# Optimization experiments

Hardware: AMD Instinct MI355X
Metric: run time of the kernel (lower is better)

The kernel has to match this reference:

```python
import jax, jax.numpy as jnp
import numpy as np

N_SPECIES = 2
N_RBF = 16
HIDDEN = 64
CUTOFF = 2.5


def setup_inputs() -> dict:
    key = jax.random.key(0)
    ks = jax.random.split(key, 10)
    B, N = 8, 1024
    positions = jax.random.uniform(ks[0], (B, N, 3), dtype=jnp.float32) * 10.0
    types = jax.random.randint(ks[1], (B, N), 0, N_SPECIES)
    in_dim = N_SPECIES + N_SPECIES * N_RBF  # 34
    def lin(k, fan_in, fan_out):
        bound = 1.0 / np.sqrt(fan_in)
        kw, kb = jax.random.split(k)
        W = jax.random.uniform(kw, (fan_in, fan_out), minval=-bound, maxval=bound, dtype=jnp.float32)
        b = jax.random.uniform(kb, (fan_out,), minval=-bound, maxval=bound, dtype=jnp.float32)
        return W, b
    W1, b1 = lin(ks[2], in_dim, 64)
    W2, b2 = lin(ks[3], 64, 64)
    W3, b3 = lin(ks[4], 64, HIDDEN)
    return {"positions": positions, "types": types,
            "W1": W1, "b1": b1, "W2": W2, "b2": b2, "W3": W3, "b3": b3}


def _forward(positions, types, W1, b1, W2, b2, W3, b3):
    B, N, _ = positions.shape
    # pairwise distances with safe sqrt (zero grad on diagonal, matching torch norm subgradient)
    disp = positions[:, :, None, :] - positions[:, None, :, :]          # [B,N,N,3]
    sq = jnp.sum(disp * disp, axis=-1)                                   # [B,N,N]
    nz = sq > 0.0
    d = jnp.sqrt(jnp.where(nz, sq, 1.0)) * nz
    # RBF expansion
    centers = jnp.linspace(0.0, CUTOFF, N_RBF)
    widths = jnp.full((N_RBF,), CUTOFF / max(N_RBF - 1, 1))
    diff = d[..., None] - centers                                        # [B,N,N,R]
    rbf = jnp.exp(-(diff ** 2) / (widths ** 2 + 1e-12))
    # smooth polynomial cutoff
    x = d / CUTOFF
    cut = jnp.where(d < CUTOFF, 1.0 - 6.0 * x ** 5 + 15.0 * x ** 4 - 10.0 * x ** 3, 0.0)
    rbf = rbf * cut[..., None]
    eye = jnp.eye(N, dtype=bool)[None, :, :, None]
    rbf = jnp.where(eye, 0.0, rbf)
    # species-weighted neighbor aggregation
    onehot = jax.nn.one_hot(types, N_SPECIES, dtype=positions.dtype)      # [B,N,S]
    env = jnp.einsum('bijr,bjs->birs', rbf, onehot).reshape(B, N, -1)     # [B,N,R*S]
    feats = jnp.concatenate([onehot, env], axis=-1)                       # [B,N,S+S*R]
    h = jax.nn.silu(feats @ W1 + b1)
    h = jax.nn.silu(h @ W2 + b2)
    return h @ W3 + b3                                                    # [B,N,HIDDEN]


def reference(positions, types, W1, b1, W2, b2, W3, b3):
    return _forward(positions, types, W1, b1, W2, b2, W3, b3)
```

## Files before the change

### kernel.cpp

```cpp
#include <hip/hip_runtime.h>
#include <hip/hip_bf16.h>

#define NTHREADS 256
#define N_ATOMS 1024
#define HIDDEN 64

__device__ __forceinline__ float rdlane(float v, int l) {
    return __int_as_float(__builtin_amdgcn_readlane(__float_as_int(v), l));
}

__global__ __launch_bounds__(NTHREADS) void LocalFeatureEncoder_40063454937486_kernel(
    const float* __restrict__ pos,
    const int*   __restrict__ types,
    const float* __restrict__ W1,
    const float* __restrict__ b1,
    const float* __restrict__ W2,
    const float* __restrict__ b2,
    const float* __restrict__ W3,
    const float* __restrict__ b3,
    float*       __restrict__ out)
{
    const int tid  = threadIdx.x;
    const int lane = tid & 63;
    const int a    = blockIdx.x * 4 + (tid >> 6);
    const int bidx = a >> 10;
    const int i    = a & (N_ATOMS - 1);

    const float* posb = pos + (size_t)bidx * N_ATOMS * 3;
    const int*   typb = types + (size_t)bidx * N_ATOMS;

    const float xi = posb[i * 3 + 0];
    const float yi = posb[i * 3 + 1];
    const float zi = posb[i * 3 + 2];

    const int   r16 = lane & 15;
    const int   slot = lane >> 4;
    const float c    = (float)r16 * (2.5f / 15.0f);

    float acc0 = 0.0f;
    float acc1 = 0.0f;

#pragma unroll
    for (int sweep = 0; sweep < N_ATOMS / 64; ++sweep) {
        const int j = lane + sweep * 64;
        const float px = posb[j * 3 + 0];
        const float py = posb[j * 3 + 1];
        const float pz = posb[j * 3 + 2];
        const int   tj = typb[j];
        const float dx = xi - px, dy = yi - py, dz = zi - pz;
        const float sq = dx * dx + dy * dy + dz * dz;
        const bool  pred = (j != i) && (sq < 6.25f);

        float dv = 0.0f, mp = 0.0f;
        if (pred) {
            const float d  = sqrtf(sq);
            const float x  = d * 0.4f;
            const float x3 = x * x * x;
            const float cutv = 1.0f + x3 * (-10.0f + x * (15.0f - 6.0f * x));
            dv = d;
            mp = (tj == 0) ? cutv : -cutv;
        }

        unsigned long long mask = __ballot(pred);
        while (mask) {
            float dA = 0.0f, mA = 0.0f, dB = 0.0f, mB = 0.0f;
            float dC = 0.0f, mC = 0.0f, dD = 0.0f, mD = 0.0f;
            {
                const int s = __builtin_ctzll(mask); mask &= mask - 1;
                dA = rdlane(dv, s); mA = rdlane(mp, s);
            }
            if (mask) {
                const int s = __builtin_ctzll(mask); mask &= mask - 1;
                dB = rdlane(dv, s); mB = rdlane(mp, s);
            }
            if (mask) {
                const int s = __builtin_ctzll(mask); mask &= mask - 1;
                dC = rdlane(dv, s); mC = rdlane(mp, s);
            }
            if (mask) {
                const int s = __builtin_ctzll(mask); mask &= mask - 1;
                dD = rdlane(dv, s); mD = rdlane(mp, s);
            }
            const float d = (slot == 0) ? dA : (slot == 1) ? dB : (slot == 2) ? dC : dD;
            const float m = (slot == 0) ? mA : (slot == 1) ? mB : (slot == 2) ? mC : dD == dD ? mD : mD;
            const float diff = d - c;
            const float e = __expf(diff * diff * -36.0f);
            acc0 += e * fmaxf(m, 0.0f);
            acc1 += e * fmaxf(-m, 0.0f);
        }
    }

    acc0 += __shfl_xor(acc0, 16, 64);
    acc0 += __shfl_xor(acc0, 32, 64);
    acc1 += __shfl_xor(acc1, 16, 64);
    acc1 += __shfl_xor(acc1, 32, 64);

    const int t  = lane;
    const int ti = typb[i];

    float h1 = b1[t] + W1[ti * HIDDEN + t];
#pragma unroll
    for (int r = 0; r < 16; ++r) {
        h1 += rdlane(acc0, r) * W1[(2 + 2 * r + 0) * HIDDEN + t];
        h1 += rdlane(acc1, r) * W1[(2 + 2 * r + 1) * HIDDEN + t];
    }
    h1 = h1 / (1.0f + __expf(-h1));

    float h2 = b2[t];
#pragma unroll
    for (int k = 0; k < HIDDEN; ++k) {
        h2 += rdlane(h1, k) * W2[k * HIDDEN + t];
    }
    h2 = h2 / (1.0f + __expf(-h2));

    float o = b3[t];
#pragma unroll
    for (int k = 0; k < HIDDEN; ++k) {
        o += rdlane(h2, k) * W3[k * HIDDEN + t];
    }
    out[(size_t)a * HIDDEN + t] = o;
}

extern "C" void kernel_launch(void* const* d_in, const int* in_sizes, int n_in,
                              void* d_out, int out_size, void* d_ws, size_t ws_size,
                              hipStream_t stream) {
    const float* pos   = (const float*)d_in[0];
    const int*   types = (const int*)d_in[1];
    const float* W1    = (const float*)d_in[2];
    const float* b1    = (const float*)d_in[3];
    const float* W2    = (const float*)d_in[4];
    const float* b2    = (const float*)d_in[5];
    const float* W3    = (const float*)d_in[6];
    const float* b3    = (const float*)d_in[7];
    float*       out   = (float*)d_out;

    const int BN = in_sizes[1];

    LocalFeatureEncoder_40063454937486_kernel<<<BN / 4, NTHREADS, 0, stream>>>(
        pos, types, W1, b1, W2, b2, W3, b3, out);
}
```

Measured before the change: 95.55 us.

## Split env and MLP kernels, stage positions in LDS, compact neighbors via queue

Splits the fused kernel into two. The first stages the batch's positions (as SoA) and type signs in shared memory and compacts neighbor (distance, signed cutoff) pairs into a per-wave LDS queue using prefix popcount, replacing the serial readlane loop. It writes 36-float features to workspace. The second kernel computes the three-layer MLP for tiles of 32 atoms with the weights staged in shared memory, so weight loads are reused across atoms. The split costs a second launch, a workspace round trip, and each block redundantly loading a full batch's positions into LDS.

```diff
diff --git a/kernel.cpp b/kernel.cpp
--- a/kernel.cpp
+++ b/kernel.cpp
@@ -1,92 +1,92 @@
 #include <hip/hip_runtime.h>
 #include <hip/hip_bf16.h>
 
-#define NTHREADS 256
 #define N_ATOMS 1024
-#define HIDDEN 64
-
-__device__ __forceinline__ float rdlane(float v, int l) {
-    return __int_as_float(__builtin_amdgcn_readlane(__float_as_int(v), l));
-}
-
-__global__ __launch_bounds__(NTHREADS) void LocalFeatureEncoder_40063454937486_kernel(
+#define HIDDEN  64
+#define TM      32
+#define FSTRIDE 36
+#define QCAP    67
+
+__global__ __launch_bounds__(256) void k1_env(
     const float* __restrict__ pos,
     const int*   __restrict__ types,
-    const float* __restrict__ W1,
-    const float* __restrict__ b1,
-    const float* __restrict__ W2,
-    const float* __restrict__ b2,
-    const float* __restrict__ W3,
-    const float* __restrict__ b3,
-    float*       __restrict__ out)
+    float*       __restrict__ ws)
 {
     const int tid  = threadIdx.x;
     const int lane = tid & 63;
-    const int a    = blockIdx.x * 4 + (tid >> 6);
+    const int wav  = tid >> 6;
+    const int a    = blockIdx.x * 4 + wav;
     const int bidx = a >> 10;
     const int i    = a & (N_ATOMS - 1);
 
-    const float* posb = pos + (size_t)bidx * N_ATOMS * 3;
-    const int*   typb = types + (size_t)bidx * N_ATOMS;
-
-    const float xi = posb[i * 3 + 0];
-    const float yi = posb[i * 3 + 1];
-    const float zi = posb[i * 3 + 2];
-
-    const int   r16 = lane & 15;
+    __shared__ float sdat[4 * N_ATOMS];
+    __shared__ float qbuf[4 * QCAP * 2];
+
+    {
+        const float* pf = pos + (size_t)bidx * (N_ATOMS * 3);
+#pragma unroll
+        for (int rep = 0; rep < 3; ++rep) {
+            const int f0 = rep * 1024 + tid * 4;
+            const float4 v = *(const float4*)(pf + f0);
+#pragma unroll
+            for (int q = 0; q < 4; ++q) {
+                const int f  = f0 + q;
+                const int j  = f / 3;
+                const int cc = f - j * 3;
+                sdat[cc * N_ATOMS + j] = (&v.x)[q];
+            }
+        }
+        const int4 tv = *(const int4*)(types + (size_t)bidx * N_ATOMS + tid * 4);
+        float4 tsv;
+        tsv.x = (tv.x == 0) ? 1.0f : -1.0f;
+        tsv.y = (tv.y == 0) ? 1.0f : -1.0f;
+        tsv.z = (tv.z == 0) ? 1.0f : -1.0f;
+        tsv.w = (tv.w == 0) ? 1.0f : -1.0f;
+        *(float4*)&sdat[3 * N_ATOMS + tid * 4] = tsv;
+    }
+    __syncthreads();
+
+    const float xi = sdat[i];
+    const float yi = sdat[N_ATOMS + i];
+    const float zi = sdat[2 * N_ATOMS + i];
+
     const int   slot = lane >> 4;
+    const int   r16  = lane & 15;
     const float c    = (float)r16 * (2.5f / 15.0f);
+    const int   qb   = wav * (QCAP * 2);
 
     float acc0 = 0.0f;
     float acc1 = 0.0f;
 
-#pragma unroll
-    for (int sweep = 0; sweep < N_ATOMS / 64; ++sweep) {
-        const int j = lane + sweep * 64;
-        const float px = posb[j * 3 + 0];
-        const float py = posb[j * 3 + 1];
-        const float pz = posb[j * 3 + 2];
-        const int   tj = typb[j];
+    for (int s = 0; s < N_ATOMS / 64; ++s) {
+        const int jj = lane + s * 64;
+        const float px  = sdat[jj];
+        const float py  = sdat[N_ATOMS + jj];
+        const float pz  = sdat[2 * N_ATOMS + jj];
+        const float tsj = sdat[3 * N_ATOMS + jj];
         const float dx = xi - px, dy = yi - py, dz = zi - pz;
         const float sq = dx * dx + dy * dy + dz * dz;
-        const bool  pred = (j != i) && (sq < 6.25f);
-
-        float dv = 0.0f, mp = 0.0f;
+        const bool pred = (jj != i) && (sq < 6.25f);
+
+        const unsigned long long mask = __ballot(pred);
+        const int ns = (int)__popcll(mask);
+
         if (pred) {
             const float d  = sqrtf(sq);
             const float x  = d * 0.4f;
             const float x3 = x * x * x;
             const float cutv = 1.0f + x3 * (-10.0f + x * (15.0f - 6.0f * x));
-            dv = d;
-            mp = (tj == 0) ? cutv : -cutv;
-        }
-
-        unsigned long long mask = __ballot(pred);
-        while (mask) {
-            float dA = 0.0f, mA = 0.0f, dB = 0.0f, mB = 0.0f;
-            float dC = 0.0f, mC = 0.0f, dD = 0.0f, mD = 0.0f;
-            {
-                const int s = __builtin_ctzll(mask); mask &= mask - 1;
-                dA = rdlane(dv, s); mA = rdlane(mp, s);
-            }
-            if (mask) {
-                const int s = __builtin_ctzll(mask); mask &= mask - 1;
-                dB = rdlane(dv, s); mB = rdlane(mp, s);
-            }
-            if (mask) {
-                const int s = __builtin_ctzll(mask); mask &= mask - 1;
-                dC = rdlane(dv, s); mC = rdlane(mp, s);
-            }
-            if (mask) {
-                const int s = __builtin_ctzll(mask); mask &= mask - 1;
-                dD = rdlane(dv, s); mD = rdlane(mp, s);
-            }
-            const float d = (slot == 0) ? dA : (slot == 1) ? dB : (slot == 2) ? dC : dD;
-            const float m = (slot == 0) ? mA : (slot == 1) ? mB : (slot == 2) ? mC : dD == dD ? mD : mD;
-            const float diff = d - c;
-            const float e = __expf(diff * diff * -36.0f);
-            acc0 += e * fmaxf(m, 0.0f);
-            acc1 += e * fmaxf(-m, 0.0f);
+            const int idx = (int)__popcll(mask & ((1ull << lane) - 1ull));
+            *(float2*)&qbuf[qb + idx * 2] = make_float2(d, cutv * tsj);
+        }
+        if (lane < 3) *(float2*)&qbuf[qb + (ns + lane) * 2] = make_float2(0.0f, 0.0f);
+
+        for (int e = 0; e < ns; e += 4) {
+            const float2 dm = *(const float2*)&qbuf[qb + (e + slot) * 2];
+            const float diff = dm.x - c;
+            const float ex = __expf(diff * diff * -36.0f);
+            acc0 += ex * fmaxf(dm.y, 0.0f);
+            acc1 += ex * fmaxf(-dm.y, 0.0f);
         }
     }
 
@@ -95,30 +95,96 @@
     acc1 += __shfl_xor(acc1, 16, 64);
     acc1 += __shfl_xor(acc1, 32, 64);
 
-    const int t  = lane;
-    const int ti = typb[i];
-
-    float h1 = b1[t] + W1[ti * HIDDEN + t];
-#pragma unroll
-    for (int r = 0; r < 16; ++r) {
-        h1 += rdlane(acc0, r) * W1[(2 + 2 * r + 0) * HIDDEN + t];
-        h1 += rdlane(acc1, r) * W1[(2 + 2 * r + 1) * HIDDEN + t];
-    }
-    h1 = h1 / (1.0f + __expf(-h1));
-
-    float h2 = b2[t];
-#pragma unroll
-    for (int k = 0; k < HIDDEN; ++k) {
-        h2 += rdlane(h1, k) * W2[k * HIDDEN + t];
-    }
-    h2 = h2 / (1.0f + __expf(-h2));
-
-    float o = b3[t];
-#pragma unroll
-    for (int k = 0; k < HIDDEN; ++k) {
-        o += rdlane(h2, k) * W3[k * HIDDEN + t];
-    }
-    out[(size_t)a * HIDDEN + t] = o;
+    const float tsi = sdat[3 * N_ATOMS + i];
+    const int   ti  = (tsi < 0.0f) ? 1 : 0;
+
+    float* wsa = ws + (size_t)a * FSTRIDE;
+    if (lane < 2)  wsa[lane] = (ti == lane) ? 1.0f : 0.0f;
+    if (lane < 16) *(float2*)&wsa[2 + 2 * lane] = make_float2(acc0, acc1);
+}
+
+__global__ __launch_bounds__(256) void k2_mlp(
+    const float* __restrict__ ws,
+    const float* __restrict__ W1, const float* __restrict__ b1,
+    const float* __restrict__ W2, const float* __restrict__ b2,
+    const float* __restrict__ W3, const float* __restrict__ b3,
+    float*       __restrict__ out)
+{
+    const int tid = threadIdx.x;
+    const int t   = tid & 63;
+    const int g   = tid >> 6;
+    const int a0  = blockIdx.x * TM;
+
+    __shared__ float w[64 * 64];
+    __shared__ float actA[TM * 64];
+    __shared__ float actB[TM * 64];
+
+    for (int idx = tid; idx < TM * FSTRIDE; idx += 256) {
+        const int m = idx / FSTRIDE;
+        const int k = idx - m * FSTRIDE;
+        actA[m * 64 + k] = ws[(size_t)a0 * FSTRIDE + idx];
+    }
+    for (int idx = tid; idx < 34 * 64; idx += 256) w[idx] = W1[idx];
+    __syncthreads();
+
+    float acc[8];
+
+    {
+        const float bias = b1[t];
+#pragma unroll
+        for (int j = 0; j < 8; ++j) acc[j] = bias;
+        for (int k = 0; k < 34; ++k) {
+            const float wv = w[k * 64 + t];
+#pragma unroll
+            for (int j = 0; j < 8; ++j)
+                acc[j] += actA[(g * 8 + j) * 64 + k] * wv;
+        }
+    }
+    __syncthreads();
+#pragma unroll
+    for (int j = 0; j < 8; ++j) {
+        float h = acc[j];
+        h = h / (1.0f + __expf(-h));
+        actB[(g * 8 + j) * 64 + t] = h;
+    }
+    for (int idx = tid; idx < 64 * 64; idx += 256) w[idx] = W2[idx];
+    __syncthreads();
+
+    {
+        const float bias = b2[t];
+#pragma unroll
+        for (int j = 0; j < 8; ++j) acc[j] = bias;
+        for (int k = 0; k < 64; ++k) {
+            const float wv = w[k * 64 + t];
+#pragma unroll
+            for (int j = 0; j < 8; ++j)
+                acc[j] += actB[(g * 8 + j) * 64 + k] * wv;
+        }
+    }
+    __syncthreads();
+#pragma unroll
+    for (int j = 0; j < 8; ++j) {
+        float h = acc[j];
+        h = h / (1.0f + __expf(-h));
+        actA[(g * 8 + j) * 64 + t] = h;
+    }
+    for (int idx = tid; idx < 64 * 64; idx += 256) w[idx] = W3[idx];
+    __syncthreads();
+
+    {
+        const float bias = b3[t];
+#pragma unroll
+        for (int j = 0; j < 8; ++j) acc[j] = bias;
+        for (int k = 0; k < 64; ++k) {
+            const float wv = w[k * 64 + t];
+#pragma unroll
+            for (int j = 0; j < 8; ++j)
+                acc[j] += actA[(g * 8 + j) * 64 + k] * wv;
+        }
+#pragma unroll
+        for (int j = 0; j < 8; ++j)
+            out[(size_t)(a0 + g * 8 + j) * HIDDEN + t] = acc[j];
+    }
 }
 
 extern "C" void kernel_launch(void* const* d_in, const int* in_sizes, int n_in,
@@ -133,9 +199,10 @@
     const float* W3    = (const float*)d_in[6];
     const float* b3    = (const float*)d_in[7];
     float*       out   = (float*)d_out;
+    float*       feats = (float*)d_ws;
 
     const int BN = in_sizes[1];
 
-    LocalFeatureEncoder_40063454937486_kernel<<<BN / 4, NTHREADS, 0, stream>>>(
-        pos, types, W1, b1, W2, b2, W3, b3, out);
+    k1_env<<<BN / 4, 256, 0, stream>>>(pos, types, feats);
+    k2_mlp<<<BN / TM, 256, 0, stream>>>(feats, W1, b1, W2, b2, W3, b3, out);
 }
```

Measured after the change: 99.96 us. 1.05x slower.
